# Performance work log

Hardware: AMD Instinct MI355X
Metric: run time of the kernel (lower is better)

Reference implementation:

```python
import jax, jax.numpy as jnp
import numpy as np

N = 50000      # nodes
E = 800000     # edges (before self-loops)
IN = 128       # in_channels
HID = 32       # hidden_channels
H = 4          # heads (hidden layers)
H_LAST = 6     # heads of final conv (concat=False -> mean)
OUT = 2        # out_channels
NEG = 0.2      # LeakyReLU slope in GATConv


def setup_inputs() -> dict:
    key = jax.random.key(0)
    ks = jax.random.split(key, 24)
    r = lambda k, s, sc=0.1: (jax.random.normal(k, s, jnp.float32) * sc)
    inp = {
        "x": jax.random.normal(ks[0], (N, IN), jnp.float32),
        "edge_index": jax.random.randint(ks[1], (2, E), 0, N, dtype=jnp.int32),
        "edge_attr": jax.random.normal(ks[2], (E, 1), jnp.float32),  # ignored by GATConv (edge_dim=None)
        # layer 0: GATConv(IN -> HID, heads=H, concat) + Linear(IN -> HID*H)
        "c0_W": r(ks[3], (IN, H * HID)), "c0_as": r(ks[4], (H, HID)), "c0_ad": r(ks[5], (H, HID)), "c0_b": jnp.zeros((H * HID,), jnp.float32),
        "l0_W": r(ks[6], (IN, H * HID)), "l0_b": jnp.zeros((H * HID,), jnp.float32),
        # layer 1 (middle): GATConv(HID*H -> HID, heads=H) + Linear(HID*H -> HID*H)
        "c1_W": r(ks[7], (H * HID, H * HID)), "c1_as": r(ks[8], (H, HID)), "c1_ad": r(ks[9], (H, HID)), "c1_b": jnp.zeros((H * HID,), jnp.float32),
        "l1_W": r(ks[10], (H * HID, H * HID)), "l1_b": jnp.zeros((H * HID,), jnp.float32),
        # layer 2 (last): GATConv(HID*H -> OUT, heads=H_LAST, concat=False) + Linear(HID*H -> OUT)
        "c2_W": r(ks[11], (H * HID, H_LAST * OUT)), "c2_as": r(ks[12], (H_LAST, OUT)), "c2_ad": r(ks[13], (H_LAST, OUT)), "c2_b": jnp.zeros((OUT,), jnp.float32),
        "l2_W": r(ks[14], (H * HID, OUT)), "l2_b": jnp.zeros((OUT,), jnp.float32),
    }
    return inp


def gat_conv(x, src, dst, W, a_src, a_dst, b, heads, ch, concat):
    n = x.shape[0]
    xw = (x @ W).reshape(n, heads, ch)                      # [N,H,C]
    al_s = jnp.einsum('nhc,hc->nh', xw, a_src)              # [N,H]
    al_d = jnp.einsum('nhc,hc->nh', xw, a_dst)
    alpha = jax.nn.leaky_relu(al_s[src] + al_d[dst], NEG)   # [E,H]
    # segment softmax over edges sharing the same destination node
    m = jax.ops.segment_max(alpha, dst, num_segments=n)
    e = jnp.exp(alpha - m[dst])
    s = jax.ops.segment_sum(e, dst, num_segments=n)
    coef = e / s[dst]                                       # [E,H]
    out = jax.ops.segment_sum(xw[src] * coef[:, :, None], dst, num_segments=n)  # [N,H,C]
    out = out.reshape(n, heads * ch) if concat else out.mean(axis=1)
    return out + b


def reference(x, edge_index, edge_attr,
              c0_W, c0_as, c0_ad, c0_b, l0_W, l0_b,
              c1_W, c1_as, c1_ad, c1_b, l1_W, l1_b,
              c2_W, c2_as, c2_ad, c2_b, l2_W, l2_b):
    n = x.shape[0]
    loops = jnp.arange(n, dtype=edge_index.dtype)  # GATConv add_self_loops=True
    src = jnp.concatenate([edge_index[0], loops])
    dst = jnp.concatenate([edge_index[1], loops])
    # edge_attr is ignored: GATConv built without edge_dim has lin_edge=None
    h = jax.nn.relu(gat_conv(x, src, dst, c0_W, c0_as, c0_ad, c0_b, H, HID, True) + x @ l0_W + l0_b)
    h = jax.nn.relu(gat_conv(h, src, dst, c1_W, c1_as, c1_ad, c1_b, H, HID, True) + h @ l1_W + l1_b)
    out = gat_conv(h, src, dst, c2_W, c2_as, c2_ad, c2_b, H_LAST, OUT, False) + h @ l2_W + l2_b
    return out
```

## Files before the change

kernel.cpp:

```cpp
#include <hip/hip_runtime.h>
#include <hip/hip_bf16.h>


#define NEG_SLOPE 0.2f
#define SC_CHUNK 4096
#define CAP 64

typedef __attribute__((ext_vector_type(8))) short short8;
typedef __attribute__((ext_vector_type(4))) float floatx4;

static __device__ __forceinline__ float leaky(float x) {
    return x > 0.f ? x : NEG_SLOPE * x;
}

static __device__ __forceinline__ unsigned short f2bf(float f) {
    unsigned int u = __float_as_uint(f);
    u = (u + 0x7fffu + ((u >> 16) & 1u)) >> 16;
    return (unsigned short)u;
}

static __device__ __forceinline__ unsigned int pack_bf2(float lo, float hi) {
    return (unsigned int)f2bf(lo) | ((unsigned int)f2bf(hi) << 16);
}

static __device__ __forceinline__ float bflo(unsigned int u) {
    return __uint_as_float(u << 16);
}
static __device__ __forceinline__ float bfhi(unsigned int u) {
    return __uint_as_float(u & 0xffff0000u);
}

static __device__ __forceinline__ short8 frag_from_f32(const float* p) {
    float4 f0 = ((const float4*)p)[0];
    float4 f1 = ((const float4*)p)[1];
    short8 r;
    r[0] = (short)f2bf(f0.x); r[1] = (short)f2bf(f0.y);
    r[2] = (short)f2bf(f0.z); r[3] = (short)f2bf(f0.w);
    r[4] = (short)f2bf(f1.x); r[5] = (short)f2bf(f1.y);
    r[6] = (short)f2bf(f1.z); r[7] = (short)f2bf(f1.w);
    return r;
}

__global__ __launch_bounds__(256) void k_bucket(
    const int* __restrict__ ei, int E, int N, int rs,
    int* __restrict__ cnt, int* __restrict__ col,
    const float* __restrict__ W0, unsigned short* __restrict__ T0,
    const float* __restrict__ W1, unsigned short* __restrict__ T1,
    const float* __restrict__ W2, unsigned short* __restrict__ T2,
    const float* __restrict__ W3, unsigned short* __restrict__ T3,
    const float* __restrict__ c2W, const float* __restrict__ l2W,
    unsigned short* __restrict__ WT5) {
    if (blockIdx.y == gridDim.y - 1) {
        int tid = blockIdx.x * 256 + threadIdx.x;
        for (int j = tid; j < 65536; j += 2048) {
            int wsel = j >> 14, t = j & 16383;
            int n = t >> 7, k = t & 127;
            const float* W = (wsel == 0) ? W0 : (wsel == 1) ? W1 : (wsel == 2) ? W2 : W3;
            unsigned short* T = (wsel == 0) ? T0 : (wsel == 1) ? T1 : (wsel == 2) ? T2 : T3;
            T[n * 128 + k] = f2bf(W[k * 128 + n]);
        }
        {
            int n = tid >> 7, k = tid & 127;
            float v = 0.f;
            if (n < 12) v = c2W[k * 12 + n];
            else if (n < 14) v = l2W[k * 2 + (n - 12)];
            WT5[n * 128 + k] = f2bf(v);
        }
        return;
    }
    int lo = blockIdx.x * rs, hi = lo + rs;
    int base = blockIdx.y * SC_CHUNK;
    int ET = E + N;
#pragma unroll 4
    for (int o = threadIdx.x; o < SC_CHUNK; o += 256) {
        int e = base + o;
        if (e >= ET) break;
        int d = (e < E) ? ei[E + e] : (e - E);
        if (d < lo || d >= hi) continue;
        int s = (e < E) ? ei[e] : d;
        int pos = atomicAdd(&cnt[d], 1);
        if (pos < CAP) col[(d << 6) + pos] = s;
    }
}

__global__ __launch_bounds__(256) void k_gemm_mfma(
    const float* __restrict__ x0,
    const unsigned short* __restrict__ Ab,
    const unsigned short* __restrict__ W1T,
    unsigned int* __restrict__ XWb,
    const float* __restrict__ a_s, const float* __restrict__ a_d,
    float4* __restrict__ ALS4, float4* __restrict__ ALD4,
    const unsigned short* __restrict__ W2T,
    const float* __restrict__ b2,
    unsigned short* __restrict__ Hsb,
    int M) {
    __shared__ short8 Wl[128 * 17];
    int which = blockIdx.y;
    const short8* W8 = (const short8*)(which ? W2T : W1T);

    for (int u = threadIdx.x; u < 2048; u += 256)
        Wl[(u >> 4) * 17 + (u & 15)] = W8[u];

    int w = threadIdx.x >> 6, lane = threadIdx.x & 63;
    int m = lane & 15, q = lane >> 4;
    const short8* A8 = (const short8*)Ab;

    short8 af[2][4];
    int rt0 = blockIdx.x * 8 + w;
#pragma unroll
    for (int t = 0; t < 2; t++) {
        int arow = (rt0 + t * 4) * 16 + m;
        int lrow = (arow < M) ? arow : (M - 1);
#pragma unroll
        for (int ks = 0; ks < 4; ks++) {
            af[t][ks] = x0 ? frag_from_f32(x0 + (size_t)lrow * 128 + (ks * 4 + q) * 8)
                           : A8[arow * 16 + ks * 4 + q];
        }
    }
    __syncthreads();

#pragma unroll
    for (int t = 0; t < 2; t++) {
        floatx4 acc[8];
#pragma unroll
        for (int ct = 0; ct < 8; ct++) acc[ct] = (floatx4){0.f, 0.f, 0.f, 0.f};
#pragma unroll
        for (int ks = 0; ks < 4; ks++) {
#pragma unroll
            for (int ct = 0; ct < 8; ct++) {
                short8 bfrag = Wl[(ct * 16 + m) * 17 + ks * 4 + q];
                acc[ct] = __builtin_amdgcn_mfma_f32_16x16x32_bf16(af[t][ks], bfrag, acc[ct], 0, 0, 0);
            }
        }

        int crow0 = (rt0 + t * 4) * 16 + q * 4;
        if (which) {
#pragma unroll
            for (int ct = 0; ct < 8; ct++) {
                int gc = ct * 16 + m;
                float bias = b2[gc];
#pragma unroll
                for (int r = 0; r < 4; r++) {
                    int gr = crow0 + r;
                    if (gr < M) Hsb[gr * 128 + gc] = f2bf(acc[ct][r] + bias);
                }
            }
        } else {
#pragma unroll
            for (int ct = 0; ct < 4; ct++) {
#pragma unroll
                for (int r = 0; r < 4; r++) {
                    int gr = crow0 + r;
                    if (gr < M)
                        XWb[gr * 64 + ct * 16 + m] = pack_bf2(acc[ct][r], acc[ct + 4][r]);
                }
            }
            float sv[4][4], dv[4][4];
#pragma unroll
            for (int h = 0; h < 4; h++) {
                float as0 = a_s[h * 32 + m], as1 = a_s[h * 32 + 16 + m];
                float ad0 = a_d[h * 32 + m], ad1 = a_d[h * 32 + 16 + m];
#pragma unroll
                for (int r = 0; r < 4; r++) {
                    sv[h][r] = acc[2 * h][r] * as0 + acc[2 * h + 1][r] * as1;
                    dv[h][r] = acc[2 * h][r] * ad0 + acc[2 * h + 1][r] * ad1;
                }
            }
#pragma unroll
            for (int off = 8; off >= 1; off >>= 1) {
#pragma unroll
                for (int h = 0; h < 4; h++)
#pragma unroll
                    for (int r = 0; r < 4; r++) {
                        sv[h][r] += __shfl_xor(sv[h][r], off);
                        dv[h][r] += __shfl_xor(dv[h][r], off);
                    }
            }
            if (m == 0) {
#pragma unroll
                for (int r = 0; r < 4; r++) {
                    int gr = crow0 + r;
                    if (gr < M) {
                        ALS4[gr] = make_float4(sv[0][r], sv[1][r], sv[2][r], sv[3][r]);
                        ALD4[gr] = make_float4(dv[0][r], dv[1][r], dv[2][r], dv[3][r]);
                    }
                }
            }
        }
    }
}

__global__ __launch_bounds__(256) void k_gemm_small(
    const unsigned short* __restrict__ Ab,
    const unsigned short* __restrict__ WT5,
    const float* __restrict__ c2as, const float* __restrict__ c2ad,
    const float* __restrict__ l2b,
    float* __restrict__ L2D, float* __restrict__ ALD2,
    float* __restrict__ out, int M) {
    int w = threadIdx.x >> 6, lane = threadIdx.x & 63;
    int m = lane & 15, q = lane >> 4;
    const short8* A8 = (const short8*)Ab;
    const short8* W8 = (const short8*)WT5;
    floatx4 acc = (floatx4){0.f, 0.f, 0.f, 0.f};
    int arow = blockIdx.x * 64 + w * 16 + m;
#pragma unroll
    for (int ks = 0; ks < 4; ks++) {
        short8 afrag = A8[arow * 16 + ks * 4 + q];
        short8 bfrag = W8[m * 16 + ks * 4 + q];
        acc = __builtin_amdgcn_mfma_f32_16x16x32_bf16(afrag, bfrag, acc, 0, 0, 0);
    }
    float asm_ = (m < 12) ? c2as[m] : 0.f;
    float adm  = (m < 12) ? c2ad[m] : 0.f;
    int crow0 = blockIdx.x * 64 + w * 16 + q * 4;
    float sc[4], dc[4];
#pragma unroll
    for (int r = 0; r < 4; r++) {
        sc[r] = acc[r] * asm_;
        dc[r] = acc[r] * adm;
    }
#pragma unroll
    for (int r = 0; r < 4; r++) {
        sc[r] += __shfl_xor(sc[r], 1);
        dc[r] += __shfl_xor(dc[r], 1);
    }
#pragma unroll
    for (int r = 0; r < 4; r++) {
        int gr = crow0 + r;
        if (gr >= M) continue;
        if (m < 12) {
            L2D[gr * 20 + m] = acc[r];
            if ((m & 1) == 0) {
                int h = m >> 1;
                L2D[gr * 20 + 12 + h] = sc[r];
                ALD2[gr * 8 + h] = dc[r];
            }
        } else if (m == 12) {
            out[gr * 2 + 0] = acc[r] + l2b[0];
        } else if (m == 13) {
            out[gr * 2 + 1] = acc[r] + l2b[1];
        }
    }
}

__global__ __launch_bounds__(256) void k_agg4(
    const int* __restrict__ cntv, const int* __restrict__ col,
    const uint4* __restrict__ XWb4,
    const float4* __restrict__ ALS4, const float4* __restrict__ ALD4,
    const float* __restrict__ cb,
    const unsigned short* __restrict__ Hsb, unsigned short* __restrict__ Hb, int N) {
    int wid = threadIdx.x >> 6, lane = threadIdx.x & 63;
    int node = blockIdx.x * 4 + wid;
    if (node >= N) return;
    int deg = cntv[node];
    if (deg > CAP) deg = CAP;
    int start = node << 6;
    int gq = lane >> 4, g = lane & 15;
    int hA = g >> 3;
    int cval = col[start + lane];
    float4 cl = ((const float4*)cb)[g];
    float4 ch = ((const float4*)cb)[g + 16];
    uint2 skl = ((const uint2*)(Hsb + node * 128))[g];
    uint2 skh = ((const uint2*)(Hsb + node * 128 + 64))[g];
    float4 ad = ALD4[node];
    float adA = hA ? ad.y : ad.x;
    float adB = hA ? ad.w : ad.z;

    float a0 = 0.f, a1 = 0.f, a2 = 0.f, a3 = 0.f;
    float b0 = 0.f, b1 = 0.f, b2 = 0.f, b3 = 0.f;
    float sA = 0.f, sB = 0.f;

#define QUAD(qq)                                                        \
    bool t##qq; float4 as##qq; uint4 u##qq;                             \
    {                                                                   \
        int idx = (qq) * 4 + gq;                                        \
        t##qq = idx < deg;                                              \
        int sv = __shfl(cval, t##qq ? idx : 0);                         \
        as##qq = ALS4[sv];                                              \
        u##qq = XWb4[(size_t)sv * 16 + g];                              \
    }

#define CQ(qq)                                                          \
    {                                                                   \
        float eA = t##qq ? __expf(leaky((hA ? as##qq.y : as##qq.x) + adA)) : 0.f; \
        float eB = t##qq ? __expf(leaky((hA ? as##qq.w : as##qq.z) + adB)) : 0.f; \
        sA += eA; sB += eB;                                             \
        a0 += eA * bflo(u##qq.x); b0 += eB * bfhi(u##qq.x);             \
        a1 += eA * bflo(u##qq.y); b1 += eB * bfhi(u##qq.y);             \
        a2 += eA * bflo(u##qq.z); b2 += eB * bfhi(u##qq.z);             \
        a3 += eA * bflo(u##qq.w); b3 += eB * bfhi(u##qq.w);             \
    }

    if (deg <= 16) {
        QUAD(0) QUAD(1) QUAD(2) QUAD(3)
        CQ(0) CQ(1) CQ(2) CQ(3)
    } else if (deg <= 24) {
        QUAD(0) QUAD(1) QUAD(2) QUAD(3) QUAD(4) QUAD(5)
        CQ(0) CQ(1) CQ(2) CQ(3) CQ(4) CQ(5)
    } else {
        QUAD(0) QUAD(1) QUAD(2) QUAD(3) QUAD(4) QUAD(5) QUAD(6) QUAD(7)
        CQ(0) CQ(1) CQ(2) CQ(3) CQ(4) CQ(5) CQ(6) CQ(7)
        for (int i = 32; i < deg; i += 4) {
            int idx = i + gq;
            bool tt = idx < deg;
            int sv = __shfl(cval, tt ? idx : 0);
            float4 as = ALS4[sv];
            uint4 uu = XWb4[(size_t)sv * 16 + g];
            float eA = tt ? __expf(leaky((hA ? as.y : as.x) + adA)) : 0.f;
            float eB = tt ? __expf(leaky((hA ? as.w : as.z) + adB)) : 0.f;
            sA += eA; sB += eB;
            a0 += eA * bflo(uu.x); b0 += eB * bfhi(uu.x);
            a1 += eA * bflo(uu.y); b1 += eB * bfhi(uu.y);
            a2 += eA * bflo(uu.z); b2 += eB * bfhi(uu.z);
            a3 += eA * bflo(uu.w); b3 += eB * bfhi(uu.w);
        }
    }
#undef QUAD
#undef CQ

#define RED2(v) { v += __shfl_xor(v, 16); v += __shfl_xor(v, 32); }
    RED2(sA) RED2(sB)
    RED2(a0) RED2(a1) RED2(a2) RED2(a3)
    RED2(b0) RED2(b1) RED2(b2) RED2(b3)
#undef RED2

    if (gq == 0) {
        float invA = 1.f / sA, invB = 1.f / sB;
        float v0 = a0 * invA + cl.x + bflo(skl.x);
        float v1 = a1 * invA + cl.y + bfhi(skl.x);
        float v2 = a2 * invA + cl.z + bflo(skl.y);
        float v3 = a3 * invA + cl.w + bfhi(skl.y);
        float w0 = b0 * invB + ch.x + bflo(skh.x);
        float w1 = b1 * invB + ch.y + bfhi(skh.x);
        float w2 = b2 * invB + ch.z + bflo(skh.y);
        float w3 = b3 * invB + ch.w + bfhi(skh.y);
        v0 = v0 > 0.f ? v0 : 0.f;  v1 = v1 > 0.f ? v1 : 0.f;
        v2 = v2 > 0.f ? v2 : 0.f;  v3 = v3 > 0.f ? v3 : 0.f;
        w0 = w0 > 0.f ? w0 : 0.f;  w1 = w1 > 0.f ? w1 : 0.f;
        w2 = w2 > 0.f ? w2 : 0.f;  w3 = w3 > 0.f ? w3 : 0.f;
        uint2 ol, oh;
        ol.x = pack_bf2(v0, v1); ol.y = pack_bf2(v2, v3);
        oh.x = pack_bf2(w0, w1); oh.y = pack_bf2(w2, w3);
        ((uint2*)(Hb + node * 128))[g] = ol;
        ((uint2*)(Hb + node * 128 + 64))[g] = oh;
    }
}

__global__ __launch_bounds__(256) void k_agg2(
    const int* __restrict__ cntv, const int* __restrict__ col,
    const float4* __restrict__ L2D4,
    const float* __restrict__ ALD2,
    const float* __restrict__ c2b,
    float* __restrict__ out, int N) {
    int g = threadIdx.x >> 4, l = threadIdx.x & 15;
    int node = blockIdx.x * 16 + g;
    if (node >= N) return;
    int deg = cntv[node];
    if (deg > CAP) deg = CAP;
    int start = node << 6;

    float m0 = (l      < deg) ? 1.f : 0.f;
    float m1 = (l + 16 < deg) ? 1.f : 0.f;
    float m2 = (l + 32 < deg) ? 1.f : 0.f;
    float m3 = (l + 48 < deg) ? 1.f : 0.f;
    int s0 = col[start + ((l      < deg) ? l      : 0)];
    int s1 = col[start + ((l + 16 < deg) ? l + 16 : 0)];
    int s2 = col[start + ((l + 32 < deg) ? l + 32 : 0)];
    int s3 = col[start + ((l + 48 < deg) ? l + 48 : 0)];

    float ald[6];
    {
        float4 d03 = *(const float4*)(ALD2 + node * 8);
        float2 d45 = *(const float2*)(ALD2 + node * 8 + 4);
        ald[0] = d03.x; ald[1] = d03.y; ald[2] = d03.z; ald[3] = d03.w;
        ald[4] = d45.x; ald[5] = d45.y;
    }

#define LOADN(k, sv)                                                       \
    float4 xA##k = L2D4[(size_t)(sv) * 5 + 0];                             \
    float4 xB##k = L2D4[(size_t)(sv) * 5 + 1];                             \
    float4 xC##k = L2D4[(size_t)(sv) * 5 + 2];                             \
    float4 aS##k = L2D4[(size_t)(sv) * 5 + 3];                             \
    float4 aT##k = L2D4[(size_t)(sv) * 5 + 4];
    LOADN(0, s0) LOADN(1, s1) LOADN(2, s2) LOADN(3, s3)
#undef LOADN

    float se[6], a0[6], a1[6];
#pragma unroll
    for (int h = 0; h < 6; h++) { se[h] = 0.f; a0[h] = 0.f; a1[h] = 0.f; }

#define COMPN(k, mk)                                                       \
    {                                                                      \
        float als[6] = {aS##k.x, aS##k.y, aS##k.z, aS##k.w, aT##k.x, aT##k.y}; \
        float xw[12] = {xA##k.x, xA##k.y, xA##k.z, xA##k.w,                \
                        xB##k.x, xB##k.y, xB##k.z, xB##k.w,                \
                        xC##k.x, xC##k.y, xC##k.z, xC##k.w};               \
        _Pragma("unroll")                                                  \
        for (int h = 0; h < 6; h++) {                                      \
            float e = (mk) * __expf(leaky(als[h] + ald[h]));               \
            se[h] += e;                                                    \
            a0[h] += e * xw[2 * h];                                        \
            a1[h] += e * xw[2 * h + 1];                                    \
        }                                                                  \
    }
    COMPN(0, m0) COMPN(1, m1) COMPN(2, m2) COMPN(3, m3)
#undef COMPN

#pragma unroll
    for (int m = 8; m >= 1; m >>= 1) {
#pragma unroll
        for (int h = 0; h < 6; h++) {
            se[h] += __shfl_xor(se[h], m);
            a0[h] += __shfl_xor(a0[h], m);
            a1[h] += __shfl_xor(a1[h], m);
        }
    }
    if (l == 0) {
        float o0 = 0.f, o1 = 0.f;
#pragma unroll
        for (int h = 0; h < 6; h++) {
            float inv = 1.f / se[h];
            o0 += a0[h] * inv;
            o1 += a1[h] * inv;
        }
        out[node * 2 + 0] += o0 * (1.f / 6.f) + c2b[0];
        out[node * 2 + 1] += o1 * (1.f / 6.f) + c2b[1];
    }
}


extern "C" void kernel_launch(void* const* d_in, const int* in_sizes, int n_in,
                              void* d_out, int out_size, void* d_ws, size_t ws_size,
                              hipStream_t stream) {
    const float* x   = (const float*)d_in[0];
    const int* ei    = (const int*)d_in[1];
    const float* c0W = (const float*)d_in[3];
    const float* c0as = (const float*)d_in[4];
    const float* c0ad = (const float*)d_in[5];
    const float* c0b = (const float*)d_in[6];
    const float* l0W = (const float*)d_in[7];
    const float* l0b = (const float*)d_in[8];
    const float* c1W = (const float*)d_in[9];
    const float* c1as = (const float*)d_in[10];
    const float* c1ad = (const float*)d_in[11];
    const float* c1b = (const float*)d_in[12];
    const float* l1W = (const float*)d_in[13];
    const float* l1b = (const float*)d_in[14];
    const float* c2W = (const float*)d_in[15];
    const float* c2as = (const float*)d_in[16];
    const float* c2ad = (const float*)d_in[17];
    const float* c2b = (const float*)d_in[18];
    const float* l2W = (const float*)d_in[19];
    const float* l2b = (const float*)d_in[20];
    float* out = (float*)d_out;

    const int N = in_sizes[0] / 128;
    const int E = in_sizes[1] / 2;
    const int ET = E + N;
    const int Mpad = (N + 63) & ~63;

    char* p = (char*)d_ws;
    auto alloc = [&](size_t bytes) -> void* {
        void* r = (void*)p;
        p += (bytes + 255) & ~(size_t)255;
        return r;
    };
    unsigned short* Hsb = (unsigned short*)alloc((size_t)N * 128 * 2);
    unsigned int* XWb = (unsigned int*)alloc((size_t)N * 64 * 4);
    unsigned short* Ab = (unsigned short*)alloc((size_t)Mpad * 128 * 2);
    unsigned short* W1T = (unsigned short*)alloc(128 * 128 * 2);
    unsigned short* W2T = (unsigned short*)alloc(128 * 128 * 2);
    unsigned short* W3T = (unsigned short*)alloc(128 * 128 * 2);
    unsigned short* W4T = (unsigned short*)alloc(128 * 128 * 2);
    unsigned short* WT5 = (unsigned short*)alloc(16 * 128 * 2);
    float* ALS = (float*)alloc((size_t)N * 4 * 4);
    float* ALD = (float*)alloc((size_t)N * 8 * 4);
    float* L2D = (float*)alloc((size_t)N * 20 * 4);
    int* cnt    = (int*)alloc((size_t)N * 4);
    int* col    = (int*)alloc((size_t)N * CAP * 4);

    hipMemsetAsync(cnt, 0, (size_t)N * 4, stream);
    int rs = (N + 7) / 8;
    int chunks = (ET + SC_CHUNK - 1) / SC_CHUNK;
    dim3 bgrid(8, chunks + 1);
    k_bucket<<<bgrid, 256, 0, stream>>>(ei, E, N, rs, cnt, col,
                                        c0W, W1T, l0W, W2T, c1W, W3T, l1W, W4T,
                                        c2W, l2W, WT5);

    dim3 ggrid((Mpad + 127) / 128, 2);
    int nwb = (N + 3) / 4;

    k_gemm_mfma<<<ggrid, 256, 0, stream>>>(x, Ab, W1T, XWb, c0as, c0ad,
                                           (float4*)ALS, (float4*)ALD,
                                           W2T, l0b, Hsb, N);
    k_agg4<<<nwb, 256, 0, stream>>>(cnt, col, (const uint4*)XWb,
                                    (const float4*)ALS, (const float4*)ALD,
                                    c0b, Hsb, Ab, N);

    k_gemm_mfma<<<ggrid, 256, 0, stream>>>(nullptr, Ab, W3T, XWb, c1as, c1ad,
                                           (float4*)ALS, (float4*)ALD,
                                           W4T, l1b, Hsb, N);
    k_agg4<<<nwb, 256, 0, stream>>>(cnt, col, (const uint4*)XWb,
                                    (const float4*)ALS, (const float4*)ALD,
                                    c1b, Hsb, Ab, N);

    k_gemm_small<<<Mpad / 64, 256, 0, stream>>>(Ab, WT5, c2as, c2ad, l2b,
                                                L2D, ALD, out, N);
    k_agg2<<<(N + 15) / 16, 256, 0, stream>>>(cnt, col, (const float4*)L2D,
                                              ALD, c2b, out, N);
}
```

Baseline: 309.6 us.

## Fuse edge bucketing with first-layer GEMM into one launch

Weight conversion moves into a small separate kernel. The edge bucketing blocks and the layer-0 GEMM blocks are merged into one kernel launch, with the block index selecting the role. This lets the independent scatter (atomic-bound) and GEMM work overlap on the GPU instead of running back to back, at the cost of an extra tiny convert launch and larger shared memory per bucket block.

```diff
diff --git a/kernel.cpp b/kernel.cpp
--- a/kernel.cpp
+++ b/kernel.cpp
@@ -41,50 +41,168 @@
     return r;
 }
 
-__global__ __launch_bounds__(256) void k_bucket(
-    const int* __restrict__ ei, int E, int N, int rs,
-    int* __restrict__ cnt, int* __restrict__ col,
+__global__ __launch_bounds__(256) void k_convert(
     const float* __restrict__ W0, unsigned short* __restrict__ T0,
     const float* __restrict__ W1, unsigned short* __restrict__ T1,
     const float* __restrict__ W2, unsigned short* __restrict__ T2,
     const float* __restrict__ W3, unsigned short* __restrict__ T3,
     const float* __restrict__ c2W, const float* __restrict__ l2W,
     unsigned short* __restrict__ WT5) {
-    if (blockIdx.y == gridDim.y - 1) {
-        int tid = blockIdx.x * 256 + threadIdx.x;
-        for (int j = tid; j < 65536; j += 2048) {
-            int wsel = j >> 14, t = j & 16383;
-            int n = t >> 7, k = t & 127;
-            const float* W = (wsel == 0) ? W0 : (wsel == 1) ? W1 : (wsel == 2) ? W2 : W3;
-            unsigned short* T = (wsel == 0) ? T0 : (wsel == 1) ? T1 : (wsel == 2) ? T2 : T3;
-            T[n * 128 + k] = f2bf(W[k * 128 + n]);
-        }
-        {
-            int n = tid >> 7, k = tid & 127;
-            float v = 0.f;
-            if (n < 12) v = c2W[k * 12 + n];
-            else if (n < 14) v = l2W[k * 2 + (n - 12)];
-            WT5[n * 128 + k] = f2bf(v);
+    int tid = blockIdx.x * 256 + threadIdx.x;
+    for (int j = tid; j < 65536; j += 2048) {
+        int wsel = j >> 14, t = j & 16383;
+        int n = t >> 7, k = t & 127;
+        const float* W = (wsel == 0) ? W0 : (wsel == 1) ? W1 : (wsel == 2) ? W2 : W3;
+        unsigned short* T = (wsel == 0) ? T0 : (wsel == 1) ? T1 : (wsel == 2) ? T2 : T3;
+        T[n * 128 + k] = f2bf(W[k * 128 + n]);
+    }
+    {
+        int n = tid >> 7, k = tid & 127;
+        float v = 0.f;
+        if (n < 12) v = c2W[k * 12 + n];
+        else if (n < 14) v = l2W[k * 2 + (n - 12)];
+        WT5[n * 128 + k] = f2bf(v);
+    }
+}
+
+static __device__ __forceinline__ void gemm_body(
+    const float* __restrict__ x0, const unsigned short* __restrict__ Ab,
+    const short8* __restrict__ W8,
+    unsigned int* __restrict__ XWb,
+    const float* __restrict__ a_s, const float* __restrict__ a_d,
+    float4* __restrict__ ALS4, float4* __restrict__ ALD4,
+    const float* __restrict__ b2, unsigned short* __restrict__ Hsb,
+    int M, int which, int bx, short8* Wl, int tid) {
+    for (int u = tid; u < 2048; u += 256)
+        Wl[(u >> 4) * 17 + (u & 15)] = W8[u];
+
+    int w = tid >> 6, lane = tid & 63;
+    int m = lane & 15, q = lane >> 4;
+    const short8* A8 = (const short8*)Ab;
+
+    short8 af[2][4];
+    int rt0 = bx * 8 + w;
+#pragma unroll
+    for (int t = 0; t < 2; t++) {
+        int arow = (rt0 + t * 4) * 16 + m;
+        int lrow = (arow < M) ? arow : (M - 1);
+#pragma unroll
+        for (int ks = 0; ks < 4; ks++) {
+            af[t][ks] = x0 ? frag_from_f32(x0 + (size_t)lrow * 128 + (ks * 4 + q) * 8)
+                           : A8[arow * 16 + ks * 4 + q];
+        }
+    }
+    __syncthreads();
+
+#pragma unroll
+    for (int t = 0; t < 2; t++) {
+        floatx4 acc[8];
+#pragma unroll
+        for (int ct = 0; ct < 8; ct++) acc[ct] = (floatx4){0.f, 0.f, 0.f, 0.f};
+#pragma unroll
+        for (int ks = 0; ks < 4; ks++) {
+#pragma unroll
+            for (int ct = 0; ct < 8; ct++) {
+                short8 bfrag = Wl[(ct * 16 + m) * 17 + ks * 4 + q];
+                acc[ct] = __builtin_amdgcn_mfma_f32_16x16x32_bf16(af[t][ks], bfrag, acc[ct], 0, 0, 0);
+            }
+        }
+
+        int crow0 = (rt0 + t * 4) * 16 + q * 4;
+        if (which) {
+#pragma unroll
+            for (int ct = 0; ct < 8; ct++) {
+                int gc = ct * 16 + m;
+                float bias = b2[gc];
+#pragma unroll
+                for (int r = 0; r < 4; r++) {
+                    int gr = crow0 + r;
+                    if (gr < M) Hsb[gr * 128 + gc] = f2bf(acc[ct][r] + bias);
+                }
+            }
+        } else {
+#pragma unroll
+            for (int ct = 0; ct < 4; ct++) {
+#pragma unroll
+                for (int r = 0; r < 4; r++) {
+                    int gr = crow0 + r;
+                    if (gr < M)
+                        XWb[gr * 64 + ct * 16 + m] = pack_bf2(acc[ct][r], acc[ct + 4][r]);
+                }
+            }
+            float sv[4][4], dv[4][4];
+#pragma unroll
+            for (int h = 0; h < 4; h++) {
+                float as0 = a_s[h * 32 + m], as1 = a_s[h * 32 + 16 + m];
+                float ad0 = a_d[h * 32 + m], ad1 = a_d[h * 32 + 16 + m];
+#pragma unroll
+                for (int r = 0; r < 4; r++) {
+                    sv[h][r] = acc[2 * h][r] * as0 + acc[2 * h + 1][r] * as1;
+                    dv[h][r] = acc[2 * h][r] * ad0 + acc[2 * h + 1][r] * ad1;
+                }
+            }
+#pragma unroll
+            for (int off = 8; off >= 1; off >>= 1) {
+#pragma unroll
+                for (int h = 0; h < 4; h++)
+#pragma unroll
+                    for (int r = 0; r < 4; r++) {
+                        sv[h][r] += __shfl_xor(sv[h][r], off);
+                        dv[h][r] += __shfl_xor(dv[h][r], off);
+                    }
+            }
+            if (m == 0) {
+#pragma unroll
+                for (int r = 0; r < 4; r++) {
+                    int gr = crow0 + r;
+                    if (gr < M) {
+                        ALS4[gr] = make_float4(sv[0][r], sv[1][r], sv[2][r], sv[3][r]);
+                        ALD4[gr] = make_float4(dv[0][r], dv[1][r], dv[2][r], dv[3][r]);
+                    }
+                }
+            }
+        }
+    }
+}
+
+__global__ __launch_bounds__(256) void k_fused0(
+    const int* __restrict__ ei, int E, int N, int rs, int nbucket, int gx,
+    int* __restrict__ cnt, int* __restrict__ col,
+    const float* __restrict__ x0,
+    const unsigned short* __restrict__ W1T,
+    unsigned int* __restrict__ XWb,
+    const float* __restrict__ a_s, const float* __restrict__ a_d,
+    float4* __restrict__ ALS4, float4* __restrict__ ALD4,
+    const unsigned short* __restrict__ W2T,
+    const float* __restrict__ b2,
+    unsigned short* __restrict__ Hsb, int M) {
+    __shared__ short8 Wl[128 * 17];
+    int b = blockIdx.x;
+    if (b < nbucket) {
+        int range = b & 7, chunk = b >> 3;
+        int lo = range * rs, hi = lo + rs;
+        int base = chunk * SC_CHUNK;
+        int ET = E + N;
+#pragma unroll 4
+        for (int o = threadIdx.x; o < SC_CHUNK; o += 256) {
+            int e = base + o;
+            if (e >= ET) break;
+            int d = (e < E) ? ei[E + e] : (e - E);
+            if (d < lo || d >= hi) continue;
+            int s = (e < E) ? ei[e] : d;
+            int pos = atomicAdd(&cnt[d], 1);
+            if (pos < CAP) col[(d << 6) + pos] = s;
         }
         return;
     }
-    int lo = blockIdx.x * rs, hi = lo + rs;
-    int base = blockIdx.y * SC_CHUNK;
-    int ET = E + N;
-#pragma unroll 4
-    for (int o = threadIdx.x; o < SC_CHUNK; o += 256) {
-        int e = base + o;
-        if (e >= ET) break;
-        int d = (e < E) ? ei[E + e] : (e - E);
-        if (d < lo || d >= hi) continue;
-        int s = (e < E) ? ei[e] : d;
-        int pos = atomicAdd(&cnt[d], 1);
-        if (pos < CAP) col[(d << 6) + pos] = s;
-    }
+    int gid = b - nbucket;
+    int which = (gid >= gx) ? 1 : 0;
+    int bx = which ? (gid - gx) : gid;
+    gemm_body(x0, nullptr, (const short8*)(which ? W2T : W1T),
+              XWb, a_s, a_d, ALS4, ALD4, b2, Hsb, M, which, bx, Wl, threadIdx.x);
 }
 
 __global__ __launch_bounds__(256) void k_gemm_mfma(
-    const float* __restrict__ x0,
     const unsigned short* __restrict__ Ab,
     const unsigned short* __restrict__ W1T,
     unsigned int* __restrict__ XWb,
@@ -92,102 +210,12 @@
     float4* __restrict__ ALS4, float4* __restrict__ ALD4,
     const unsigned short* __restrict__ W2T,
     const float* __restrict__ b2,
-    unsigned short* __restrict__ Hsb,
-    int M) {
+    unsigned short* __restrict__ Hsb, int M) {
     __shared__ short8 Wl[128 * 17];
     int which = blockIdx.y;
-    const short8* W8 = (const short8*)(which ? W2T : W1T);
-
-    for (int u = threadIdx.x; u < 2048; u += 256)
-        Wl[(u >> 4) * 17 + (u & 15)] = W8[u];
-
-    int w = threadIdx.x >> 6, lane = threadIdx.x & 63;
-    int m = lane & 15, q = lane >> 4;
-    const short8* A8 = (const short8*)Ab;
-
-    short8 af[2][4];
-    int rt0 = blockIdx.x * 8 + w;
-#pragma unroll
-    for (int t = 0; t < 2; t++) {
-        int arow = (rt0 + t * 4) * 16 + m;
-        int lrow = (arow < M) ? arow : (M - 1);
-#pragma unroll
-        for (int ks = 0; ks < 4; ks++) {
-            af[t][ks] = x0 ? frag_from_f32(x0 + (size_t)lrow * 128 + (ks * 4 + q) * 8)
-                           : A8[arow * 16 + ks * 4 + q];
-        }
-    }
-    __syncthreads();
-
-#pragma unroll
-    for (int t = 0; t < 2; t++) {
-        floatx4 acc[8];
-#pragma unroll
-        for (int ct = 0; ct < 8; ct++) acc[ct] = (floatx4){0.f, 0.f, 0.f, 0.f};
-#pragma unroll
-        for (int ks = 0; ks < 4; ks++) {
-#pragma unroll
-            for (int ct = 0; ct < 8; ct++) {
-                short8 bfrag = Wl[(ct * 16 + m) * 17 + ks * 4 + q];
-                acc[ct] = __builtin_amdgcn_mfma_f32_16x16x32_bf16(af[t][ks], bfrag, acc[ct], 0, 0, 0);
-            }
-        }
-
-        int crow0 = (rt0 + t * 4) * 16 + q * 4;
-        if (which) {
-#pragma unroll
-            for (int ct = 0; ct < 8; ct++) {
-                int gc = ct * 16 + m;
-                float bias = b2[gc];
-#pragma unroll
-                for (int r = 0; r < 4; r++) {
-                    int gr = crow0 + r;
-                    if (gr < M) Hsb[gr * 128 + gc] = f2bf(acc[ct][r] + bias);
-                }
-            }
-        } else {
-#pragma unroll
-            for (int ct = 0; ct < 4; ct++) {
-#pragma unroll
-                for (int r = 0; r < 4; r++) {
-                    int gr = crow0 + r;
-                    if (gr < M)
-                        XWb[gr * 64 + ct * 16 + m] = pack_bf2(acc[ct][r], acc[ct + 4][r]);
-                }
-            }
-            float sv[4][4], dv[4][4];
-#pragma unroll
-            for (int h = 0; h < 4; h++) {
-                float as0 = a_s[h * 32 + m], as1 = a_s[h * 32 + 16 + m];
-                float ad0 = a_d[h * 32 + m], ad1 = a_d[h * 32 + 16 + m];
-#pragma unroll
-                for (int r = 0; r < 4; r++) {
-                    sv[h][r] = acc[2 * h][r] * as0 + acc[2 * h + 1][r] * as1;
-                    dv[h][r] = acc[2 * h][r] * ad0 + acc[2 * h + 1][r] * ad1;
-                }
-            }
-#pragma unroll
-            for (int off = 8; off >= 1; off >>= 1) {
-#pragma unroll
-                for (int h = 0; h < 4; h++)
-#pragma unroll
-                    for (int r = 0; r < 4; r++) {
-                        sv[h][r] += __shfl_xor(sv[h][r], off);
-                        dv[h][r] += __shfl_xor(dv[h][r], off);
-                    }
-            }
-            if (m == 0) {
-#pragma unroll
-                for (int r = 0; r < 4; r++) {
-                    int gr = crow0 + r;
-                    if (gr < M) {
-                        ALS4[gr] = make_float4(sv[0][r], sv[1][r], sv[2][r], sv[3][r]);
-                        ALD4[gr] = make_float4(dv[0][r], dv[1][r], dv[2][r], dv[3][r]);
-                    }
-                }
-            }
-        }
-    }
+    gemm_body(nullptr, Ab, (const short8*)(which ? W2T : W1T),
+              XWb, a_s, a_d, ALS4, ALD4, b2, Hsb, M, which, blockIdx.x,
+              Wl, threadIdx.x);
 }
 
 __global__ __launch_bounds__(256) void k_gemm_small(
@@ -479,24 +507,26 @@
     int* col    = (int*)alloc((size_t)N * CAP * 4);
 
     hipMemsetAsync(cnt, 0, (size_t)N * 4, stream);
+
+    k_convert<<<8, 256, 0, stream>>>(c0W, W1T, l0W, W2T, c1W, W3T, l1W, W4T,
+                                     c2W, l2W, WT5);
+
     int rs = (N + 7) / 8;
     int chunks = (ET + SC_CHUNK - 1) / SC_CHUNK;
-    dim3 bgrid(8, chunks + 1);
-    k_bucket<<<bgrid, 256, 0, stream>>>(ei, E, N, rs, cnt, col,
-                                        c0W, W1T, l0W, W2T, c1W, W3T, l1W, W4T,
-                                        c2W, l2W, WT5);
-
-    dim3 ggrid((Mpad + 127) / 128, 2);
+    int nbucket = 8 * chunks;
+    int gx = (Mpad + 127) / 128;
+    k_fused0<<<nbucket + 2 * gx, 256, 0, stream>>>(
+        ei, E, N, rs, nbucket, gx, cnt, col,
+        x, W1T, XWb, c0as, c0ad, (float4*)ALS, (float4*)ALD,
+        W2T, l0b, Hsb, N);
+
     int nwb = (N + 3) / 4;
-
-    k_gemm_mfma<<<ggrid, 256, 0, stream>>>(x, Ab, W1T, XWb, c0as, c0ad,
-                                           (float4*)ALS, (float4*)ALD,
-                                           W2T, l0b, Hsb, N);
     k_agg4<<<nwb, 256, 0, stream>>>(cnt, col, (const uint4*)XWb,
                                     (const float4*)ALS, (const float4*)ALD,
                                     c0b, Hsb, Ab, N);
 
-    k_gemm_mfma<<<ggrid, 256, 0, stream>>>(nullptr, Ab, W3T, XWb, c1as, c1ad,
+    dim3 ggrid(gx, 2);
+    k_gemm_mfma<<<ggrid, 256, 0, stream>>>(Ab, W3T, XWb, c1as, c1ad,
                                            (float4*)ALS, (float4*)ALD,
                                            W4T, l1b, Hsb, N);
     k_agg4<<<nwb, 256, 0, stream>>>(cnt, col, (const uint4*)XWb,
```

Measured after the change: 361.5 us. +16.7%, slower.
